# Optimization experiments

Hardware: AMD Instinct MI355X
Metric: run time of the kernel (lower is better)

Reference implementation:

```python
import math
import jax, jax.numpy as jnp
import numpy as np

B, C, L = 16, 128, 2048


def setup_inputs() -> dict:
    key = jax.random.key(0)
    kq, kk, kv, km = jax.random.split(key, 4)
    proj_query = jax.random.normal(kq, (B, C, L), dtype=jnp.float32)
    proj_key = jax.random.normal(kk, (B, C, L), dtype=jnp.float32)
    proj_val = jax.random.normal(kv, (B, C, L), dtype=jnp.float32)
    padding_mask = (jax.random.uniform(km, (B, 1, L)) > 0.1).astype(jnp.float32)
    return {
        "proj_query": proj_query,
        "proj_key": proj_key,
        "proj_val": proj_val,
        "padding_mask": padding_mask,
    }


def reference(proj_query, proj_key, proj_val, padding_mask):
    c1 = proj_query.shape[1]
    # energy: [B, Lq, Lk]
    energy = jnp.einsum("bcq,bck->bqk", proj_query, proj_key)
    attention = energy / math.sqrt(c1)
    # additive log-mask before softmax (broadcast [B,1,Lk] -> [B,Lq,Lk])
    attention = attention + jnp.log(padding_mask + 1e-6)
    attention = jax.nn.softmax(attention, axis=-1)
    # multiplicative mask after softmax
    attention = attention * padding_mask
    # out = bmm(val [B,C,Lk], attention^T [B,Lk,Lq]) -> [B,C,Lq]
    out = jnp.einsum("bck,bqk->bcq", proj_val, attention)
    return out, jnp.transpose(attention, (0, 2, 1))
```

## Files before the change

### kernel.cpp

```cpp
#include <hip/hip_runtime.h>

#define B_ 16
#define C_ 128
#define L_ 2048

typedef unsigned short u16;
typedef __bf16 bf16x8 __attribute__((ext_vector_type(8)));
typedef float floatx4 __attribute__((ext_vector_type(4)));

static __device__ __forceinline__ u16 f_to_bf16(float f) {
    union { float f; unsigned int i; } v;
    v.f = f;
    unsigned int x = v.i;
    return (u16)((x + 0x7fffu + ((x >> 16) & 1u)) >> 16);
}
static __device__ __forceinline__ bf16x8 cvt8(floatx4 a, floatx4 b) {
    union { u16 u[8]; bf16x8 v; } p;
#pragma unroll
    for (int j = 0; j < 4; ++j) { p.u[j] = f_to_bf16(a[j]); p.u[4 + j] = f_to_bf16(b[j]); }
    return p.v;
}

__global__ void k_transpose(const float* __restrict__ X, u16* __restrict__ XT) {
    int t  = blockIdx.x * blockDim.x + threadIdx.x;
    int k  = t & (L_ - 1);
    int ch = (t >> 11) & 3;
    int b  = t >> 13;
    const float* src = X + (size_t)b * C_ * L_ + (size_t)(ch * 32) * L_ + k;
    u16* dst = XT + ((size_t)b * L_ + k) * C_ + ch * 32;
    u16 v[32];
#pragma unroll
    for (int c = 0; c < 32; ++c) v[c] = f_to_bf16(src[(size_t)c * L_]);
#pragma unroll
    for (int c = 0; c < 32; c += 8) {
        union { u16 u[8]; uint4 q; } p;
#pragma unroll
        for (int j = 0; j < 8; ++j) p.u[j] = v[c + j];
        *(uint4*)(dst + c) = p.q;
    }
}

#define BM 16
#define QS 136
#define LP 136

__launch_bounds__(256, 4)
__global__ void k_fused(const float* __restrict__ Q, const u16* __restrict__ KT,
                        const float* __restrict__ V, const float* __restrict__ M,
                        float* __restrict__ PT, float* __restrict__ OUT) {
    __shared__ __attribute__((aligned(16))) u16 Qs[BM * QS];
    __shared__ __attribute__((aligned(16))) u16 LDSP[2][BM * LP];
    __shared__ float redsum[BM][4];

    const int b    = blockIdx.y;
    const int q0   = blockIdx.x * BM;
    const int tid  = threadIdx.x;
    const int lane = tid & 63;
    const int wave = tid >> 6;
    const int m16  = lane & 15;
    const int quad = lane >> 4;

    for (int i = tid; i < BM * C_; i += 256) {
        int q = i & 15, c = i >> 4;
        Qs[q * QS + c] = f_to_bf16(Q[((size_t)b * C_ + c) * L_ + q0 + q]);
    }
    __syncthreads();

    bf16x8 afr[4];
#pragma unroll
    for (int f = 0; f < 4; ++f)
        afr[f] = *(const bf16x8*)(Qs + m16 * QS + f * 32 + quad * 8);

    const u16*   ktb = KT + (size_t)b * L_ * C_;
    const float* mb  = M + (size_t)b * L_;
    const float scale = 0.08838834764831845f;

    float rs[4] = {0.f, 0.f, 0.f, 0.f};
#pragma unroll 2
    for (int t = 0; t < 32; ++t) {
        const int kh = (wave << 9) + (t << 4);
        const u16* kr = ktb + (size_t)(kh + m16) * C_ + quad * 8;
        floatx4 s = {0.f, 0.f, 0.f, 0.f};
#pragma unroll
        for (int f = 0; f < 4; ++f)
            s = __builtin_amdgcn_mfma_f32_16x16x32_bf16(afr[f], *(const bf16x8*)(kr + f * 32), s, 0, 0, 0);
        const float lm = __logf(mb[kh + m16] + 1e-6f);
#pragma unroll
        for (int r = 0; r < 4; ++r) rs[r] += __expf(fmaf(s[r], scale, lm));
    }
#pragma unroll
    for (int r = 0; r < 4; ++r) {
        float v = rs[r];
        v += __shfl_xor(v, 1, 64);
        v += __shfl_xor(v, 2, 64);
        v += __shfl_xor(v, 4, 64);
        v += __shfl_xor(v, 8, 64);
        if (m16 == 0) redsum[quad * 4 + r][wave] = v;
    }
    __syncthreads();
    float rinv[4];
#pragma unroll
    for (int r = 0; r < 4; ++r) {
        const int q = quad * 4 + r;
        rinv[r] = 1.f / (redsum[q][0] + redsum[q][1] + redsum[q][2] + redsum[q][3]);
    }

    floatx4 oacc0 = {0.f, 0.f, 0.f, 0.f};
    floatx4 oacc1 = {0.f, 0.f, 0.f, 0.f};
    float*       ptb = PT + (size_t)b * L_ * L_ + q0;
    const float* vbb = V + (size_t)b * C_ * L_;

    for (int it = 0; it < 16; ++it) {
        const int kb = it << 7;
        u16* lp = LDSP[it & 1];

#pragma unroll
        for (int half = 0; half < 2; ++half) {
            const int kl = (wave << 5) + (half << 4);
            const int kh = kb + kl;
            const u16* kr = ktb + (size_t)(kh + m16) * C_ + quad * 8;
            floatx4 s = {0.f, 0.f, 0.f, 0.f};
#pragma unroll
            for (int f = 0; f < 4; ++f)
                s = __builtin_amdgcn_mfma_f32_16x16x32_bf16(afr[f], *(const bf16x8*)(kr + f * 32), s, 0, 0, 0);
            const float mk = mb[kh + m16];
            const float lm = __logf(mk + 1e-6f);
            floatx4 po;
#pragma unroll
            for (int r = 0; r < 4; ++r) {
                const float p = __expf(fmaf(s[r], scale, lm)) * rinv[r];
                po[r] = p * mk;
            }
            *(floatx4*)(ptb + (size_t)(kh + m16) * L_ + quad * 4) = po;
#pragma unroll
            for (int r = 0; r < 4; ++r)
                lp[(quad * 4 + r) * LP + kl + m16] = f_to_bf16(po[r]);
        }
        __syncthreads();

#pragma unroll
        for (int ks = 0; ks < 4; ++ks) {
            const bf16x8 pb = *(const bf16x8*)(lp + m16 * LP + (ks << 5) + quad * 8);
            const float* va = vbb + (size_t)((wave << 5) + m16) * L_ + kb + (ks << 5) + quad * 8;
            const bf16x8 a0 = cvt8(*(const floatx4*)(va),
                                   *(const floatx4*)(va + 4));
            const bf16x8 a1 = cvt8(*(const floatx4*)(va + (size_t)16 * L_),
                                   *(const floatx4*)(va + (size_t)16 * L_ + 4));
            oacc0 = __builtin_amdgcn_mfma_f32_16x16x32_bf16(a0, pb, oacc0, 0, 0, 0);
            oacc1 = __builtin_amdgcn_mfma_f32_16x16x32_bf16(a1, pb, oacc1, 0, 0, 0);
        }
    }

    float* ob = OUT + (size_t)b * C_ * L_ + q0;
#pragma unroll
    for (int r = 0; r < 4; ++r) {
        const int c0 = (wave << 5) + (quad << 2) + r;
        ob[(size_t)c0 * L_ + m16]        = oacc0[r];
        ob[(size_t)(c0 + 16) * L_ + m16] = oacc1[r];
    }
}

extern "C" void kernel_launch(void* const* d_in, const int* in_sizes, int n_in,
                              void* d_out, int out_size, void* d_ws, size_t ws_size,
                              hipStream_t stream) {
    (void)in_sizes; (void)n_in; (void)out_size; (void)ws_size;
    const float* Q = (const float*)d_in[0];
    const float* K = (const float*)d_in[1];
    const float* V = (const float*)d_in[2];
    const float* M = (const float*)d_in[3];
    float* OUT = (float*)d_out;
    float* PT  = OUT + (size_t)B_ * C_ * L_;
    u16*   KT  = (u16*)d_ws;

    k_transpose<<<dim3((B_ * L_ * 4) / 256), dim3(256), 0, stream>>>(K, KT);
    k_fused<<<dim3(L_ / BM, B_), dim3(256), 0, stream>>>(Q, KT, V, M, PT, OUT);
}
```

Measured before the change: 751.7 us.

## Use 1024-thread blocks keeping exp scores in registers, split-K PV with tree reduction

Blocks grow to 16 waves, and each wave owns 128 keys. Each wave computes QK^T once, keeps the exponentials in registers, and reuses them for normalization instead of recomputing the QK MFMAs and exp in a second pass. Each wave then computes a partial P·V over its key slice for all 128 channels, and the partials are combined with an LDS tree reduction. A block-index swizzle remaps blocks so that consecutive ones interleave batches. This removes half of the QK work and the per-iteration barriers, at the cost of higher register pressure, a single block per CU, and extra reduction barriers.

```diff
diff --git a/kernel.cpp b/kernel.cpp
--- a/kernel.cpp
+++ b/kernel.cpp
@@ -44,23 +44,26 @@
 #define QS 136
 #define LP 136
 
-__launch_bounds__(256, 4)
+__launch_bounds__(1024, 1)
 __global__ void k_fused(const float* __restrict__ Q, const u16* __restrict__ KT,
                         const float* __restrict__ V, const float* __restrict__ M,
                         float* __restrict__ PT, float* __restrict__ OUT) {
     __shared__ __attribute__((aligned(16))) u16 Qs[BM * QS];
-    __shared__ __attribute__((aligned(16))) u16 LDSP[2][BM * LP];
-    __shared__ float redsum[BM][4];
+    __shared__ __attribute__((aligned(16))) u16 Ps[16][BM * LP];
+    __shared__ float redsum[BM][16];
 
-    const int b    = blockIdx.y;
-    const int q0   = blockIdx.x * BM;
+    const int o       = blockIdx.x;
+    const int logical = (o & 7) * 256 + (o >> 3);
+    const int b       = logical >> 7;
+    const int q0      = (logical & 127) * BM;
+
     const int tid  = threadIdx.x;
     const int lane = tid & 63;
     const int wave = tid >> 6;
     const int m16  = lane & 15;
     const int quad = lane >> 4;
 
-    for (int i = tid; i < BM * C_; i += 256) {
+    for (int i = tid; i < BM * C_; i += 1024) {
         int q = i & 15, c = i >> 4;
         Qs[q * QS + c] = f_to_bf16(Q[((size_t)b * C_ + c) * L_ + q0 + q]);
     }
@@ -75,10 +78,11 @@
     const float* mb  = M + (size_t)b * L_;
     const float scale = 0.08838834764831845f;
 
+    floatx4 accf[8];
     float rs[4] = {0.f, 0.f, 0.f, 0.f};
-#pragma unroll 2
-    for (int t = 0; t < 32; ++t) {
-        const int kh = (wave << 9) + (t << 4);
+#pragma unroll
+    for (int t = 0; t < 8; ++t) {
+        const int kh = (wave << 7) + (t << 4);
         const u16* kr = ktb + (size_t)(kh + m16) * C_ + quad * 8;
         floatx4 s = {0.f, 0.f, 0.f, 0.f};
 #pragma unroll
@@ -86,7 +90,11 @@
             s = __builtin_amdgcn_mfma_f32_16x16x32_bf16(afr[f], *(const bf16x8*)(kr + f * 32), s, 0, 0, 0);
         const float lm = __logf(mb[kh + m16] + 1e-6f);
 #pragma unroll
-        for (int r = 0; r < 4; ++r) rs[r] += __expf(fmaf(s[r], scale, lm));
+        for (int r = 0; r < 4; ++r) {
+            const float e = __expf(fmaf(s[r], scale, lm));
+            accf[t][r] = e;
+            rs[r] += e;
+        }
     }
 #pragma unroll
     for (int r = 0; r < 4; ++r) {
@@ -102,61 +110,68 @@
 #pragma unroll
     for (int r = 0; r < 4; ++r) {
         const int q = quad * 4 + r;
-        rinv[r] = 1.f / (redsum[q][0] + redsum[q][1] + redsum[q][2] + redsum[q][3]);
+        float v = redsum[q][0];
+#pragma unroll
+        for (int w = 1; w < 16; ++w) v += redsum[q][w];
+        rinv[r] = 1.f / v;
     }
 
-    floatx4 oacc0 = {0.f, 0.f, 0.f, 0.f};
-    floatx4 oacc1 = {0.f, 0.f, 0.f, 0.f};
-    float*       ptb = PT + (size_t)b * L_ * L_ + q0;
-    const float* vbb = V + (size_t)b * C_ * L_;
+    float* ptb = PT + (size_t)b * L_ * L_ + q0;
+    u16*   pw  = &Ps[wave][0];
+#pragma unroll
+    for (int t = 0; t < 8; ++t) {
+        const int kh = (wave << 7) + (t << 4);
+        const float mk = mb[kh + m16];
+        floatx4 po;
+#pragma unroll
+        for (int r = 0; r < 4; ++r) po[r] = accf[t][r] * rinv[r] * mk;
+        *(floatx4*)(ptb + (size_t)(kh + m16) * L_ + quad * 4) = po;
+#pragma unroll
+        for (int r = 0; r < 4; ++r)
+            pw[(quad * 4 + r) * LP + (t << 4) + m16] = f_to_bf16(po[r]);
+    }
 
-    for (int it = 0; it < 16; ++it) {
-        const int kb = it << 7;
-        u16* lp = LDSP[it & 1];
-
+    floatx4 acc[8];
 #pragma unroll
-        for (int half = 0; half < 2; ++half) {
-            const int kl = (wave << 5) + (half << 4);
-            const int kh = kb + kl;
-            const u16* kr = ktb + (size_t)(kh + m16) * C_ + quad * 8;
-            floatx4 s = {0.f, 0.f, 0.f, 0.f};
+    for (int ct = 0; ct < 8; ++ct) acc[ct] = (floatx4){0.f, 0.f, 0.f, 0.f};
+    const float* vbb = V + (size_t)b * C_ * L_ + (wave << 7);
 #pragma unroll
-            for (int f = 0; f < 4; ++f)
-                s = __builtin_amdgcn_mfma_f32_16x16x32_bf16(afr[f], *(const bf16x8*)(kr + f * 32), s, 0, 0, 0);
-            const float mk = mb[kh + m16];
-            const float lm = __logf(mk + 1e-6f);
-            floatx4 po;
+    for (int kt = 0; kt < 4; ++kt) {
+        const bf16x8 pb = *(const bf16x8*)(pw + m16 * LP + (kt << 5) + quad * 8);
 #pragma unroll
-            for (int r = 0; r < 4; ++r) {
-                const float p = __expf(fmaf(s[r], scale, lm)) * rinv[r];
-                po[r] = p * mk;
-            }
-            *(floatx4*)(ptb + (size_t)(kh + m16) * L_ + quad * 4) = po;
-#pragma unroll
-            for (int r = 0; r < 4; ++r)
-                lp[(quad * 4 + r) * LP + kl + m16] = f_to_bf16(po[r]);
-        }
-        __syncthreads();
-
-#pragma unroll
-        for (int ks = 0; ks < 4; ++ks) {
-            const bf16x8 pb = *(const bf16x8*)(lp + m16 * LP + (ks << 5) + quad * 8);
-            const float* va = vbb + (size_t)((wave << 5) + m16) * L_ + kb + (ks << 5) + quad * 8;
-            const bf16x8 a0 = cvt8(*(const floatx4*)(va),
-                                   *(const floatx4*)(va + 4));
-            const bf16x8 a1 = cvt8(*(const floatx4*)(va + (size_t)16 * L_),
-                                   *(const floatx4*)(va + (size_t)16 * L_ + 4));
-            oacc0 = __builtin_amdgcn_mfma_f32_16x16x32_bf16(a0, pb, oacc0, 0, 0, 0);
-            oacc1 = __builtin_amdgcn_mfma_f32_16x16x32_bf16(a1, pb, oacc1, 0, 0, 0);
+        for (int ct = 0; ct < 8; ++ct) {
+            const float* va = vbb + (size_t)((ct << 4) + m16) * L_ + (kt << 5) + quad * 8;
+            const bf16x8 a = cvt8(*(const floatx4*)(va), *(const floatx4*)(va + 4));
+            acc[ct] = __builtin_amdgcn_mfma_f32_16x16x32_bf16(a, pb, acc[ct], 0, 0, 0);
         }
     }
 
-    float* ob = OUT + (size_t)b * C_ * L_ + q0;
+    __syncthreads();
+    floatx4* red = (floatx4*)&Ps[0][0];
+    for (int half = 8; half >= 1; half >>= 1) {
+        if (wave >= half && wave < 2 * half) {
+            floatx4* slab = red + (size_t)(wave - half) * 512;
 #pragma unroll
-    for (int r = 0; r < 4; ++r) {
-        const int c0 = (wave << 5) + (quad << 2) + r;
-        ob[(size_t)c0 * L_ + m16]        = oacc0[r];
-        ob[(size_t)(c0 + 16) * L_ + m16] = oacc1[r];
+            for (int ct = 0; ct < 8; ++ct) slab[ct * 64 + lane] = acc[ct];
+        }
+        __syncthreads();
+        if (wave < half) {
+            floatx4* slab = red + (size_t)wave * 512;
+#pragma unroll
+            for (int ct = 0; ct < 8; ++ct) acc[ct] += slab[ct * 64 + lane];
+        }
+        __syncthreads();
+    }
+
+    if (wave == 0) {
+        float* ob = OUT + (size_t)b * C_ * L_ + q0;
+#pragma unroll
+        for (int ct = 0; ct < 8; ++ct) {
+            const int c0 = (ct << 4) + (quad << 2);
+#pragma unroll
+            for (int r = 0; r < 4; ++r)
+                ob[(size_t)(c0 + r) * L_ + m16] = acc[ct][r];
+        }
     }
 }
 
@@ -173,5 +188,5 @@
     u16*   KT  = (u16*)d_ws;
 
     k_transpose<<<dim3((B_ * L_ * 4) / 256), dim3(256), 0, stream>>>(K, KT);
-    k_fused<<<dim3(L_ / BM, B_), dim3(256), 0, stream>>>(Q, KT, V, M, PT, OUT);
+    k_fused<<<dim3(L_ / BM * B_), dim3(1024), 0, stream>>>(Q, KT, V, M, PT, OUT);
 }
```

Result: faster. 681.4 us (-9.3%).
